# Kernel tuning notes

Measured on AMD Instinct MI355X. Metric: run time of the kernel, lower is better.

## Reference

```python
import jax, jax.numpy as jnp
import numpy as np

TARGETS_COUNT = 8
TARGET_LEN = 256
BATCH = 32


def setup_inputs() -> dict:
    key = jax.random.key(0)
    target = jax.random.normal(key, (BATCH, TARGETS_COUNT, TARGET_LEN), dtype=jnp.float32)
    return {"target": target}


def _bispectrum(x):
    # x: [L].  TM[l1, l2] = (1/L) * sum_n x[n] * x[n-l1] * x[n-l2],
    # where x[k] = 0 for k < 0 (zero left-padding, non-circular).
    L = x.shape[0]
    n = jnp.arange(L)
    idx = n[None, :] - n[:, None]            # idx[l, n] = n - l
    S = jnp.where(idx >= 0, x[jnp.clip(idx, 0, L - 1)], jnp.float32(0))  # S[l, n] = x[n-l]
    # TM[l1, l2] = sum_n (x[n] * S[l1, n]) * S[l2, n]
    return ((S * x[None, :]) @ S.T) / L      # [L, L]


def reference(target):
    # target: [B, T, L] -> bispectrum per signal, averaged over T.
    bs = jax.vmap(jax.vmap(_bispectrum))(target)      # [B, T, L, L]
    source = jnp.mean(bs, axis=1)[:, None, :, :]       # [B, 1, L, L]
    return source, target
```

## Files before the change

### kernel.cpp

```cpp
#include <hip/hip_runtime.h>


#define LEN 256
#define NT 8
#define F1OFF 4105
#define REDSTR 68
#define SMEM_DW 8704

typedef _Float16 f16x8 __attribute__((ext_vector_type(8)));
typedef float    f32x4 __attribute__((ext_vector_type(4)));

__constant__ uchar4 kBlockTab[40] = {
    {0,0,0,0},{0,0,1,0},{0,0,2,0},{0,0,3,0},{0,0,4,0},{0,0,5,0},{0,0,6,0},{0,0,7,0},
    {1,0,2,0},{1,0,3,0},{1,0,4,0},{1,0,5,0},{1,0,6,0},{1,0,7,0},
    {1,1,2,0},{1,1,3,0},{1,1,4,0},{1,1,5,0},{1,1,6,0},{1,1,7,0},
    {2,0,4,0},{2,0,5,0},{2,0,6,0},{2,0,7,0},
    {2,1,4,0},{2,1,5,0},{2,1,6,0},{2,1,7,0},
    {2,2,4,0},{2,2,5,0},{2,2,6,0},{2,2,7,0},
    {3,0,6,0},{3,0,7,0},
    {3,1,6,0},{3,1,7,0},
    {3,2,6,0},{3,2,7,0},
    {3,3,6,0},{3,3,7,0}};
__constant__ uchar4 kPairTab[10] = {
    {0,0,0,8},{1,0,8,6},{1,1,14,6},{2,0,20,4},{2,1,24,4},{2,2,28,4},
    {3,0,32,2},{3,1,34,2},{3,2,36,2},{3,3,38,2}};

static __device__ __forceinline__ void split2(float a0, float a1, uint& hb, uint& lb) {
    auto h = __builtin_amdgcn_cvt_pkrtz(a0, a1);
    float e0 = a0 - (float)h[0];
    float e1 = a1 - (float)h[1];
    auto e = __builtin_amdgcn_cvt_pkrtz(e0, e1);
    __builtin_memcpy(&hb, &h, 4);
    __builtin_memcpy(&lb, &e, 4);
}
static __device__ __forceinline__ f16x8 mkf(const uint* u) {
    f16x8 v;
    __builtin_memcpy(&v, u, 16);
    return v;
}

template <bool PARTIAL>
__global__ __launch_bounds__(256, 4) void bispec_main(const float* __restrict__ x,
                                                      float* __restrict__ dst) {
    __shared__ float fs[SMEM_DW];
    const int b = blockIdx.y, bx = blockIdx.x;

    int ti, tj, kb0, kbn;
    if (PARTIAL) {
        uchar4 e = kBlockTab[bx];
        ti = e.x; tj = e.y; kb0 = e.z; kbn = 1;
    } else {
        uchar4 e = kPairTab[bx];
        ti = e.x; tj = e.y; kb0 = 2 * ti; kbn = 8 - 2 * ti;
    }
    const int l1b = ti << 6, l2b = tj << 6;
    const int tid = threadIdx.x;
    const int w = tid >> 6, l = tid & 63, cg = l & 15, g = l >> 4;

    const float* xb = x + b * (NT * LEN);
    for (int i = tid; i < 4096; i += 256) {
        int j = i & 511;
        float v = (j >= 256) ? xb[(i >> 9) * 256 + (j - 256)] : 0.0f;
        fs[i] = v;
        fs[F1OFF + i] = v;
    }
    __syncthreads();

    const float* fW = fs + ((cg & 1) ? F1OFF : 0);

    f32x4 acc[4][4];
    #pragma unroll
    for (int mi = 0; mi < 4; ++mi)
        #pragma unroll
        for (int ni = 0; ni < 4; ++ni) acc[mi][ni] = 0.0f;

    #pragma unroll
    for (int tt = 0; tt < 2; ++tt) {
        const int t = w + tt * 4;
        const int xB0 = t * 512 + 256 + g * 8;

        for (int kp = 0; kp < kbn; ++kp) {
            const int xB = xB0 + (kb0 + kp) * 32;
            const float* pX = fs + xB;
            const float* pA = fW + (xB - l1b - cg - 48);
            const float* pB = fW + (xB - l2b - cg - 48);

            const float4 x0 = *(const float4*)(pX);
            const float4 x1 = *(const float4*)(pX + 4);
            const float xn[8] = {x0.x, x0.y, x0.z, x0.w, x1.x, x1.y, x1.z, x1.w};

            f16x8 ah[4], al[4];
            #pragma unroll
            for (int mi = 0; mi < 4; ++mi) {
                const int off = 48 - mi * 16;
                float wv[8];
                #pragma unroll
                for (int p = 0; p < 4; ++p) {
                    const float2 d = *(const float2*)(pA + off + 2 * p);
                    wv[2 * p] = d.x; wv[2 * p + 1] = d.y;
                }
                uint Ahp[4], Alp[4];
                #pragma unroll
                for (int p = 0; p < 4; ++p)
                    split2(xn[2 * p] * wv[2 * p], xn[2 * p + 1] * wv[2 * p + 1],
                           Ahp[p], Alp[p]);
                ah[mi] = mkf(Ahp); al[mi] = mkf(Alp);
            }

            #pragma unroll
            for (int ni = 0; ni < 4; ++ni) {
                const int off = 48 - ni * 16;
                float wv[8];
                #pragma unroll
                for (int p = 0; p < 4; ++p) {
                    const float2 d = *(const float2*)(pB + off + 2 * p);
                    wv[2 * p] = d.x; wv[2 * p + 1] = d.y;
                }
                uint Bhp[4], Blp[4];
                #pragma unroll
                for (int p = 0; p < 4; ++p)
                    split2(wv[2 * p], wv[2 * p + 1], Bhp[p], Blp[p]);
                const f16x8 bh = mkf(Bhp), bl = mkf(Blp);
                #pragma unroll
                for (int mi = 0; mi < 4; ++mi) {
                    acc[mi][ni] = __builtin_amdgcn_mfma_f32_16x16x32_f16(ah[mi], bh, acc[mi][ni], 0, 0, 0);
                    acc[mi][ni] = __builtin_amdgcn_mfma_f32_16x16x32_f16(ah[mi], bl, acc[mi][ni], 0, 0, 0);
                    acc[mi][ni] = __builtin_amdgcn_mfma_f32_16x16x32_f16(al[mi], bh, acc[mi][ni], 0, 0, 0);
                }
            }
        }
    }

    __syncthreads();
    float* buf0 = fs;
    float* buf1 = fs + 4352;
    if (w >= 2) {
        float* bb = (w == 2) ? buf0 : buf1;
        #pragma unroll
        for (int mi = 0; mi < 4; ++mi)
            #pragma unroll
            for (int ni = 0; ni < 4; ++ni)
                *(f32x4*)&bb[(ni * 16 + cg) * REDSTR + mi * 16 + g * 4] = acc[mi][ni];
    }
    __syncthreads();
    if (w < 2) {
        float* bb = (w == 0) ? buf0 : buf1;
        #pragma unroll
        for (int mi = 0; mi < 4; ++mi)
            #pragma unroll
            for (int ni = 0; ni < 4; ++ni)
                acc[mi][ni] += *(f32x4*)&bb[(ni * 16 + cg) * REDSTR + mi * 16 + g * 4];
    }
    __syncthreads();
    if (w == 1) {
        #pragma unroll
        for (int mi = 0; mi < 4; ++mi)
            #pragma unroll
            for (int ni = 0; ni < 4; ++ni)
                *(f32x4*)&buf0[(ni * 16 + cg) * REDSTR + mi * 16 + g * 4] = acc[mi][ni];
    }
    __syncthreads();
    if (w == 0) {
        #pragma unroll
        for (int mi = 0; mi < 4; ++mi)
            #pragma unroll
            for (int ni = 0; ni < 4; ++ni)
                acc[mi][ni] += *(f32x4*)&buf0[(ni * 16 + cg) * REDSTR + mi * 16 + g * 4];

        if (PARTIAL) {
            float* ob = dst + ((size_t)b * 40 + bx) * 4096;
            #pragma unroll
            for (int mi = 0; mi < 4; ++mi)
                #pragma unroll
                for (int ni = 0; ni < 4; ++ni)
                    #pragma unroll
                    for (int q = 0; q < 4; ++q)
                        ob[(mi * 16 + g * 4 + q) * 64 + ni * 16 + cg] = acc[mi][ni][q];
        } else {
            const float s = 1.0f / (float)(LEN * NT);
            float* ob = dst + (size_t)b * (LEN * LEN);
            #pragma unroll
            for (int mi = 0; mi < 4; ++mi)
                #pragma unroll
                for (int ni = 0; ni < 4; ++ni)
                    #pragma unroll
                    for (int q = 0; q < 4; ++q) {
                        const float v = acc[mi][ni][q] * s;
                        const int r = l1b + mi * 16 + g * 4 + q;
                        const int cc = l2b + ni * 16 + cg;
                        ob[(size_t)r * LEN + cc] = v;
                        if (ti != tj) ob[(size_t)cc * LEN + r] = v;
                    }
        }
    }
}

__global__ __launch_bounds__(256) void bispec_reduce(const float* __restrict__ ws,
                                                     float* __restrict__ out) {
    __shared__ float tile[64][65];
    const int p = blockIdx.x, b = blockIdx.y;
    uchar4 e = kPairTab[p];
    const int ii = e.x, jj = e.y, s = e.z, c = e.w;
    const float* base = ws + ((size_t)b * 40 + s) * 4096;
    float* ob = out + (size_t)b * (LEN * LEN);
    const float scale = 1.0f / (float)(LEN * NT);
    for (int k4 = threadIdx.x; k4 < 1024; k4 += 256) {
        f32x4 v = *(const f32x4*)&base[k4 * 4];
        for (int q = 1; q < c; ++q)
            v += *(const f32x4*)&base[(size_t)q * 4096 + k4 * 4];
        v *= scale;
        const int k = k4 * 4, r = k >> 6, cc = k & 63;
        tile[r][cc] = v[0]; tile[r][cc + 1] = v[1];
        tile[r][cc + 2] = v[2]; tile[r][cc + 3] = v[3];
        *(f32x4*)&ob[(size_t)(ii * 64 + r) * LEN + jj * 64 + cc] = v;
    }
    if (ii != jj) {
        __syncthreads();
        for (int k = threadIdx.x; k < 4096; k += 256) {
            const int r = k >> 6, cc = k & 63;
            ob[(size_t)(jj * 64 + r) * LEN + ii * 64 + cc] = tile[cc][r];
        }
    }
}

extern "C" void kernel_launch(void* const* d_in, const int* in_sizes, int n_in,
                              void* d_out, int out_size, void* d_ws, size_t ws_size,
                              hipStream_t stream) {
    const float* x = (const float*)d_in[0];
    float* out = (float*)d_out;

    const size_t ws_need = (size_t)32 * 40 * 4096 * sizeof(float);
    if (ws_size >= ws_need) {
        float* ws = (float*)d_ws;
        bispec_main<true><<<dim3(40, 32), dim3(256), 0, stream>>>(x, ws);
        bispec_reduce<<<dim3(10, 32), dim3(256), 0, stream>>>(ws, out);
    } else {
        bispec_main<false><<<dim3(10, 32), dim3(256), 0, stream>>>(x, out);
    }

    (void)hipMemcpyAsync(out + (size_t)32 * LEN * LEN, x,
                         (size_t)32 * NT * LEN * sizeof(float),
                         hipMemcpyDeviceToDevice, stream);
}
```

Measured before the change: 87.75 us.

## Split 64x64 tile into per-wave quadrants, drop cross-wave reduction and duplicate smem

Each of the four waves now computes its own 32x32 quadrant of the 64x64 output tile over all eight signals, instead of all waves computing the full tile over two signals each and then reducing through shared memory. This removes the multi-stage LDS reduction and its barriers, halves shared memory by dropping the padded duplicate copy of the signals, and raises the launch-bounds occupancy hint from 4 to 8. In exchange, the weight operands are loaded from LDS as scalar reads rather than float2, and the A/B fragments are rebuilt per quadrant, so operand loading and fp16 split work is duplicated across waves and bank conflicts from the removed padding may return.

Result: faster. 84.71 us (-3.5%).

```diff
diff --git a/kernel.cpp b/kernel.cpp
--- a/kernel.cpp
+++ b/kernel.cpp
@@ -3,9 +3,7 @@
 
 #define LEN 256
 #define NT 8
-#define F1OFF 4105
-#define REDSTR 68
-#define SMEM_DW 8704
+#define SMEM_DW 4104
 
 typedef _Float16 f16x8 __attribute__((ext_vector_type(8)));
 typedef float    f32x4 __attribute__((ext_vector_type(4)));
@@ -40,7 +38,7 @@
 }
 
 template <bool PARTIAL>
-__global__ __launch_bounds__(256, 4) void bispec_main(const float* __restrict__ x,
+__global__ __launch_bounds__(256, 8) void bispec_main(const float* __restrict__ x,
                                                       float* __restrict__ dst) {
     __shared__ float fs[SMEM_DW];
     const int b = blockIdx.y, bx = blockIdx.x;
@@ -56,49 +54,37 @@
     const int l1b = ti << 6, l2b = tj << 6;
     const int tid = threadIdx.x;
     const int w = tid >> 6, l = tid & 63, cg = l & 15, g = l >> 4;
+    const int qr = (w >> 1) << 5, qc = (w & 1) << 5;
 
     const float* xb = x + b * (NT * LEN);
     for (int i = tid; i < 4096; i += 256) {
         int j = i & 511;
-        float v = (j >= 256) ? xb[(i >> 9) * 256 + (j - 256)] : 0.0f;
-        fs[i] = v;
-        fs[F1OFF + i] = v;
+        fs[i] = (j >= 256) ? xb[(i >> 9) * 256 + (j - 256)] : 0.0f;
     }
     __syncthreads();
 
-    const float* fW = fs + ((cg & 1) ? F1OFF : 0);
+    f32x4 acc[2][2];
+    #pragma unroll
+    for (int mi = 0; mi < 2; ++mi)
+        #pragma unroll
+        for (int ni = 0; ni < 2; ++ni) acc[mi][ni] = 0.0f;
 
-    f32x4 acc[4][4];
-    #pragma unroll
-    for (int mi = 0; mi < 4; ++mi)
-        #pragma unroll
-        for (int ni = 0; ni < 4; ++ni) acc[mi][ni] = 0.0f;
-
-    #pragma unroll
-    for (int tt = 0; tt < 2; ++tt) {
-        const int t = w + tt * 4;
-        const int xB0 = t * 512 + 256 + g * 8;
-
-        for (int kp = 0; kp < kbn; ++kp) {
-            const int xB = xB0 + (kb0 + kp) * 32;
-            const float* pX = fs + xB;
-            const float* pA = fW + (xB - l1b - cg - 48);
-            const float* pB = fW + (xB - l2b - cg - 48);
-
-            const float4 x0 = *(const float4*)(pX);
-            const float4 x1 = *(const float4*)(pX + 4);
+    for (int kp = 0; kp < kbn; ++kp) {
+        const int kb = kb0 + kp;
+        #pragma unroll 2
+        for (int t = 0; t < NT; ++t) {
+            const int xB = t * 512 + 256 + g * 8 + kb * 32;
+            const float4 x0 = *(const float4*)&fs[xB];
+            const float4 x1 = *(const float4*)&fs[xB + 4];
             const float xn[8] = {x0.x, x0.y, x0.z, x0.w, x1.x, x1.y, x1.z, x1.w};
 
-            f16x8 ah[4], al[4];
+            f16x8 ah[2], al[2];
             #pragma unroll
-            for (int mi = 0; mi < 4; ++mi) {
-                const int off = 48 - mi * 16;
+            for (int mi = 0; mi < 2; ++mi) {
+                const int p0 = xB - l1b - qr - mi * 16 - cg;
                 float wv[8];
                 #pragma unroll
-                for (int p = 0; p < 4; ++p) {
-                    const float2 d = *(const float2*)(pA + off + 2 * p);
-                    wv[2 * p] = d.x; wv[2 * p + 1] = d.y;
-                }
+                for (int p = 0; p < 8; ++p) wv[p] = fs[p0 + p];
                 uint Ahp[4], Alp[4];
                 #pragma unroll
                 for (int p = 0; p < 4; ++p)
@@ -108,21 +94,18 @@
             }
 
             #pragma unroll
-            for (int ni = 0; ni < 4; ++ni) {
-                const int off = 48 - ni * 16;
+            for (int ni = 0; ni < 2; ++ni) {
+                const int p0 = xB - l2b - qc - ni * 16 - cg;
                 float wv[8];
                 #pragma unroll
-                for (int p = 0; p < 4; ++p) {
-                    const float2 d = *(const float2*)(pB + off + 2 * p);
-                    wv[2 * p] = d.x; wv[2 * p + 1] = d.y;
-                }
+                for (int p = 0; p < 8; ++p) wv[p] = fs[p0 + p];
                 uint Bhp[4], Blp[4];
                 #pragma unroll
                 for (int p = 0; p < 4; ++p)
                     split2(wv[2 * p], wv[2 * p + 1], Bhp[p], Blp[p]);
                 const f16x8 bh = mkf(Bhp), bl = mkf(Blp);
                 #pragma unroll
-                for (int mi = 0; mi < 4; ++mi) {
+                for (int mi = 0; mi < 2; ++mi) {
                     acc[mi][ni] = __builtin_amdgcn_mfma_f32_16x16x32_f16(ah[mi], bh, acc[mi][ni], 0, 0, 0);
                     acc[mi][ni] = __builtin_amdgcn_mfma_f32_16x16x32_f16(ah[mi], bl, acc[mi][ni], 0, 0, 0);
                     acc[mi][ni] = __builtin_amdgcn_mfma_f32_16x16x32_f16(al[mi], bh, acc[mi][ni], 0, 0, 0);
@@ -131,67 +114,30 @@
         }
     }
 
-    __syncthreads();
-    float* buf0 = fs;
-    float* buf1 = fs + 4352;
-    if (w >= 2) {
-        float* bb = (w == 2) ? buf0 : buf1;
+    if (PARTIAL) {
+        float* ob = dst + ((size_t)b * 40 + bx) * 4096;
         #pragma unroll
-        for (int mi = 0; mi < 4; ++mi)
+        for (int mi = 0; mi < 2; ++mi)
             #pragma unroll
-            for (int ni = 0; ni < 4; ++ni)
-                *(f32x4*)&bb[(ni * 16 + cg) * REDSTR + mi * 16 + g * 4] = acc[mi][ni];
-    }
-    __syncthreads();
-    if (w < 2) {
-        float* bb = (w == 0) ? buf0 : buf1;
+            for (int ni = 0; ni < 2; ++ni)
+                #pragma unroll
+                for (int q = 0; q < 4; ++q)
+                    ob[(qr + mi * 16 + g * 4 + q) * 64 + qc + ni * 16 + cg] = acc[mi][ni][q];
+    } else {
+        const float s = 1.0f / (float)(LEN * NT);
+        float* ob = dst + (size_t)b * (LEN * LEN);
         #pragma unroll
-        for (int mi = 0; mi < 4; ++mi)
+        for (int mi = 0; mi < 2; ++mi)
             #pragma unroll
-            for (int ni = 0; ni < 4; ++ni)
-                acc[mi][ni] += *(f32x4*)&bb[(ni * 16 + cg) * REDSTR + mi * 16 + g * 4];
-    }
-    __syncthreads();
-    if (w == 1) {
-        #pragma unroll
-        for (int mi = 0; mi < 4; ++mi)
-            #pragma unroll
-            for (int ni = 0; ni < 4; ++ni)
-                *(f32x4*)&buf0[(ni * 16 + cg) * REDSTR + mi * 16 + g * 4] = acc[mi][ni];
-    }
-    __syncthreads();
-    if (w == 0) {
-        #pragma unroll
-        for (int mi = 0; mi < 4; ++mi)
-            #pragma unroll
-            for (int ni = 0; ni < 4; ++ni)
-                acc[mi][ni] += *(f32x4*)&buf0[(ni * 16 + cg) * REDSTR + mi * 16 + g * 4];
-
-        if (PARTIAL) {
-            float* ob = dst + ((size_t)b * 40 + bx) * 4096;
-            #pragma unroll
-            for (int mi = 0; mi < 4; ++mi)
+            for (int ni = 0; ni < 2; ++ni)
                 #pragma unroll
-                for (int ni = 0; ni < 4; ++ni)
-                    #pragma unroll
-                    for (int q = 0; q < 4; ++q)
-                        ob[(mi * 16 + g * 4 + q) * 64 + ni * 16 + cg] = acc[mi][ni][q];
-        } else {
-            const float s = 1.0f / (float)(LEN * NT);
-            float* ob = dst + (size_t)b * (LEN * LEN);
-            #pragma unroll
-            for (int mi = 0; mi < 4; ++mi)
-                #pragma unroll
-                for (int ni = 0; ni < 4; ++ni)
-                    #pragma unroll
-                    for (int q = 0; q < 4; ++q) {
-                        const float v = acc[mi][ni][q] * s;
-                        const int r = l1b + mi * 16 + g * 4 + q;
-                        const int cc = l2b + ni * 16 + cg;
-                        ob[(size_t)r * LEN + cc] = v;
-                        if (ti != tj) ob[(size_t)cc * LEN + r] = v;
-                    }
-        }
+                for (int q = 0; q < 4; ++q) {
+                    const float v = acc[mi][ni][q] * s;
+                    const int r = l1b + qr + mi * 16 + g * 4 + q;
+                    const int cc = l2b + qc + ni * 16 + cg;
+                    ob[(size_t)r * LEN + cc] = v;
+                    if (ti != tj) ob[(size_t)cc * LEN + r] = v;
+                }
     }
 }
 
```
